# Kernel tuning notes

Hardware: AMD Instinct MI355X
Metric: run time of the kernel (lower is better)

The kernel has to match this reference:

```python
import jax, jax.numpy as jnp
import numpy as np

B, T, D, H = 4, 1024, 1024, 16
HD = D // H  # 64
EPS = 1e-5


def _layernorm(x, g, b):
    mu = jnp.mean(x, axis=-1, keepdims=True)
    var = jnp.mean(jnp.square(x - mu), axis=-1, keepdims=True)
    return (x - mu) * jax.lax.rsqrt(var + EPS) * g + b


def _apply_rope(x, cos, sin):
    # x: (B, H, T, HD); cos/sin: (T, HD//2)
    d = x.shape[-1] // 2
    x1, x2 = x[..., :d], x[..., d:]
    cos = cos[None, None]
    sin = sin[None, None]
    return jnp.concatenate([x1 * cos - x2 * sin, x1 * sin + x2 * cos], axis=-1)


def setup_inputs() -> dict:
    key = jax.random.key(0)
    ks = jax.random.split(key, 8)
    s = 0.02
    x = jax.random.normal(ks[0], (B, T, D), jnp.float32)
    # RoPE tables
    pos = jnp.arange(T, dtype=jnp.float32)
    inv_freq = 1.0 / (10000.0 ** (jnp.arange(HD // 2, dtype=jnp.float32) / (HD // 2)))
    ang = pos[:, None] * inv_freq[None, :]  # (T, HD//2)
    rope_cos, rope_sin = jnp.cos(ang), jnp.sin(ang)
    # causal mask: True = masked out (module does ~attn_mask before SDPA)
    attn_mask = jnp.triu(jnp.ones((T, T), dtype=bool), k=1)
    params = dict(
        ln1_g=jnp.ones((D,), jnp.float32), ln1_b=jnp.zeros((D,), jnp.float32),
        w_qkv=jax.random.normal(ks[1], (D, 3 * D), jnp.float32) * s,
        b_qkv=jnp.zeros((3 * D,), jnp.float32),
        w_out=jax.random.normal(ks[2], (D, D), jnp.float32) * s,
        b_out=jnp.zeros((D,), jnp.float32),
        ln2_g=jnp.ones((D,), jnp.float32), ln2_b=jnp.zeros((D,), jnp.float32),
        w1=jax.random.normal(ks[3], (D, 4 * D), jnp.float32) * s,
        b1=jnp.zeros((4 * D,), jnp.float32),
        w2=jax.random.normal(ks[4], (4 * D, D), jnp.float32) * s,
        b2=jnp.zeros((D,), jnp.float32),
    )
    return dict(x=x, attn_mask=attn_mask, rope_cos=rope_cos, rope_sin=rope_sin, **params)


def reference(x, attn_mask, rope_cos, rope_sin, ln1_g, ln1_b, w_qkv, b_qkv,
              w_out, b_out, ln2_g, ln2_b, w1, b1, w2, b2):
    b, t, d = x.shape
    h = _layernorm(x, ln1_g, ln1_b)
    qkv = (h @ w_qkv + b_qkv).reshape(b, t, 3, H, HD)
    q, k, v = jnp.transpose(qkv, (2, 0, 3, 1, 4))  # each (B, H, T, HD)
    q = _apply_rope(q, rope_cos, rope_sin)
    k = _apply_rope(k, rope_cos, rope_sin)
    scale = 1.0 / jnp.sqrt(jnp.asarray(HD, x.dtype))
    scores = jnp.einsum('bhqd,bhkd->bhqk', q, k) * scale
    allowed = ~attn_mask  # True = attend
    neg = jnp.finfo(scores.dtype).min
    scores = jnp.where(allowed[None, None], scores, neg)
    probs = jax.nn.softmax(scores, axis=-1)
    attn = jnp.einsum('bhqk,bhkd->bhqd', probs, v)
    attn = jnp.transpose(attn, (0, 2, 1, 3)).reshape(b, t, d)
    x = x + (attn @ w_out + b_out)
    h2 = _layernorm(x, ln2_g, ln2_b)
    mlp = jax.nn.gelu(h2 @ w1 + b1, approximate=False) @ w2 + b2
    return x + mlp
```

## Files before the change

### kernel.cpp

```cpp
#include <hip/hip_runtime.h>
#include <hip/hip_bf16.h>
#include <cstdint>


typedef __bf16 bf16x8_t __attribute__((ext_vector_type(8)));
typedef float  f32x4_t  __attribute__((ext_vector_type(4)));

#define MFMA16(a, b, c) __builtin_amdgcn_mfma_f32_16x16x32_bf16((a), (b), (c), 0, 0, 0)

static constexpr int Bb = 4, T = 1024, D = 1024, NH = 16, HD = 64;
static constexpr int ROWS = Bb * T;
static constexpr int QKVN = 3 * D;

__device__ __forceinline__ float bf2f(__hip_bfloat16 v) { return __bfloat162float(v); }
__device__ __forceinline__ ushort f2bfbits(float v) {
    __hip_bfloat16 h = __float2bfloat16(v);
    return *reinterpret_cast<ushort*>(&h);
}
__device__ __forceinline__ float loadf(const void* p, size_t i, int isb16) {
    return isb16 ? bf2f(((const __hip_bfloat16*)p)[i]) : ((const float*)p)[i];
}
__device__ __forceinline__ int dtype16(const void* gref) {
    return (((const unsigned*)gref)[0] & 0xFFFFu) != 0u;
}
__device__ __forceinline__ void gld_lds16(const __hip_bfloat16* g, __hip_bfloat16* l) {
    __builtin_amdgcn_global_load_lds(
        (const __attribute__((address_space(1))) void*)g,
        (__attribute__((address_space(3))) void*)l, 16, 0, 0);
}

__device__ __forceinline__ void trans_tile(const void* B, __hip_bfloat16* BT,
                                           int K, int N, int k0, int n0, int isb16) {
    __shared__ ushort t[64][65];
#pragma unroll
    for (int it = 0; it < 16; ++it) {
        int idx = threadIdx.x + it * 256;
        int r = idx >> 6, c = idx & 63;
        t[c][r] = f2bfbits(loadf(B, (size_t)(k0 + r) * N + n0 + c, isb16));
    }
    __syncthreads();
#pragma unroll
    for (int it = 0; it < 16; ++it) {
        int idx = threadIdx.x + it * 256;
        int r = idx >> 6, c = idx & 63;
        reinterpret_cast<ushort*>(BT)[(size_t)(n0 + r) * K + k0 + c] = t[r][c];
    }
}

__global__ __launch_bounds__(256) void transpose_k(const void* __restrict__ B,
                                                   __hip_bfloat16* __restrict__ BT,
                                                   const void* __restrict__ gref,
                                                   int K, int N) {
    trans_tile(B, BT, K, N, blockIdx.y * 64, blockIdx.x * 64, dtype16(gref));
}

__global__ __launch_bounds__(256) void megatrans_k(const void* w_qkv, const void* w_out,
                                                   const void* w1, const void* w2,
                                                   __hip_bfloat16* wqkvT, __hip_bfloat16* woutT,
                                                   __hip_bfloat16* w1T, __hip_bfloat16* w2T,
                                                   const void* __restrict__ gref) {
    const int isb16 = dtype16(gref);
    int bid = blockIdx.x;
    const void* src; __hip_bfloat16* dst; int K, N, l;
    if (bid < 768)       { src = w_qkv; dst = wqkvT; K = 1024; N = 3072; l = bid; }
    else if (bid < 1024) { src = w_out; dst = woutT; K = 1024; N = 1024; l = bid - 768; }
    else if (bid < 2048) { src = w1;    dst = w1T;   K = 1024; N = 4096; l = bid - 1024; }
    else                 { src = w2;    dst = w2T;   K = 4096; N = 1024; l = bid - 2048; }
    const int nb = N / 64;
    trans_tile(src, dst, K, N, (l / nb) * 64, (l % nb) * 64, isb16);
}

__global__ __launch_bounds__(256) void ln_k(const void* __restrict__ x,
                                            const void* __restrict__ g,
                                            const void* __restrict__ bt,
                                            __hip_bfloat16* __restrict__ out,
                                            const void* __restrict__ gref) {
    const int isb16 = dtype16(gref);
    const int row = blockIdx.x, tid = threadIdx.x;
    const int lane = tid & 63, w = tid >> 6;

    float v[4];
    if (isb16) {
        ushort4 raw = reinterpret_cast<const ushort4*>((const __hip_bfloat16*)x + (size_t)row * D)[tid];
        v[0] = __uint_as_float(((unsigned)raw.x) << 16);
        v[1] = __uint_as_float(((unsigned)raw.y) << 16);
        v[2] = __uint_as_float(((unsigned)raw.z) << 16);
        v[3] = __uint_as_float(((unsigned)raw.w) << 16);
    } else {
        float4 f = reinterpret_cast<const float4*>((const float*)x + (size_t)row * D)[tid];
        v[0] = f.x; v[1] = f.y; v[2] = f.z; v[3] = f.w;
    }

    float s1 = v[0] + v[1] + v[2] + v[3];
    float s2 = v[0] * v[0] + v[1] * v[1] + v[2] * v[2] + v[3] * v[3];
#pragma unroll
    for (int off = 32; off >= 1; off >>= 1) {
        s1 += __shfl_xor(s1, off, 64);
        s2 += __shfl_xor(s2, off, 64);
    }
    __shared__ float r1[4], r2[4];
    if (lane == 0) { r1[w] = s1; r2[w] = s2; }
    __syncthreads();
    float t1 = r1[0] + r1[1] + r1[2] + r1[3];
    float t2 = r2[0] + r2[1] + r2[2] + r2[3];
    float mu  = t1 * (1.0f / D);
    float var = t2 * (1.0f / D) - mu * mu;
    float rstd = rsqrtf(var + 1e-5f);

    const int c = tid * 4;
#pragma unroll
    for (int j = 0; j < 4; j++) {
        float gv = loadf(g, c + j, isb16), bv = loadf(bt, c + j, isb16);
        out[(size_t)row * D + c + j] = __float2bfloat16((v[j] - mu) * rstd * gv + bv);
    }
}

template <int MODE, bool SPLIT>
__global__ __launch_bounds__(256) void gemm_k(const __hip_bfloat16* __restrict__ A,
                                              const __hip_bfloat16* __restrict__ BT,
                                              const void* __restrict__ bias,
                                              void* __restrict__ C,
                                              const void* __restrict__ gref,
                                              int M, int N, int Kstride, int klen) {
    __shared__ __hip_bfloat16 LB[16384];

    const int tid  = threadIdx.x;
    const int lane = tid & 63, w = tid >> 6;
    const int quad = lane >> 4, l15 = lane & 15;
    const int n0 = blockIdx.x * 128, m0 = blockIdx.y * 128;
    const int wm = (w >> 1) * 64, wn = (w & 1) * 64;
    const int kbase = SPLIT ? blockIdx.z * klen : 0;

    const int srow = lane >> 2, skk = (lane & 3) * 8;
    const __hip_bfloat16* Ag = A  + (size_t)(m0 + w * 16 + srow) * Kstride + kbase + skk;
    const __hip_bfloat16* Bg = BT + (size_t)(n0 + w * 16 + srow) * Kstride + kbase + skk;
    const int lwb = (w * 16) * 32;

    f32x4_t acc[4][4] = {};

    gld_lds16(Ag,                LB + lwb);
    gld_lds16(Ag + 64 * Kstride, LB + lwb + 64 * 32);
    gld_lds16(Bg,                LB + 8192 + lwb);
    gld_lds16(Bg + 64 * Kstride, LB + 8192 + lwb + 64 * 32);
    __syncthreads();

    int p = 0;
    for (int k0 = 0; k0 < klen; k0 += 32) {
        if (k0 + 32 < klen) {
            __hip_bfloat16* An = LB + (p ^ 1) * 4096;
            __hip_bfloat16* Bn = LB + 8192 + (p ^ 1) * 4096;
            gld_lds16(Ag + k0 + 32,                An + lwb);
            gld_lds16(Ag + k0 + 32 + 64 * Kstride, An + lwb + 64 * 32);
            gld_lds16(Bg + k0 + 32,                Bn + lwb);
            gld_lds16(Bg + k0 + 32 + 64 * Kstride, Bn + lwb + 64 * 32);
        }

        const __hip_bfloat16* Ac = LB + p * 4096;
        const __hip_bfloat16* Bc = LB + 8192 + p * 4096;
        bf16x8_t af[4], bfr[4];
#pragma unroll
        for (int t = 0; t < 4; t++) {
            af[t]  = *reinterpret_cast<const bf16x8_t*>(&Ac[(wm + t * 16 + l15) * 32 + quad * 8]);
            bfr[t] = *reinterpret_cast<const bf16x8_t*>(&Bc[(wn + t * 16 + l15) * 32 + quad * 8]);
        }
#pragma unroll
        for (int i = 0; i < 4; i++)
#pragma unroll
            for (int j = 0; j < 4; j++)
                acc[i][j] = MFMA16(af[i], bfr[j], acc[i][j]);

        __syncthreads();
        p ^= 1;
    }

    __hip_bfloat16* Cb;
    if constexpr (SPLIT) {
        const int z = blockIdx.z;
        if (z == 0)      Cb = (__hip_bfloat16*)C;
        else if (z == 1) Cb = (__hip_bfloat16*)C + (size_t)M * N;
        else if (z == 2) Cb = (__hip_bfloat16*)const_cast<void*>(bias);
        else             Cb = (__hip_bfloat16*)const_cast<void*>(gref);
    } else {
        Cb = (__hip_bfloat16*)C;
    }
    const int isb16 = (MODE == 3) ? 0 : dtype16(gref);
    __hip_bfloat16* E = LB;
#pragma unroll
    for (int j = 0; j < 4; j++) {
        const int cc = wn + j * 16 + l15;
        const float bsv = (MODE == 3) ? 0.0f : loadf(bias, n0 + cc, isb16);
#pragma unroll
        for (int i = 0; i < 4; i++) {
            const int rbase = wm + i * 16 + quad * 4;
#pragma unroll
            for (int r = 0; r < 4; r++) {
                const int rr = rbase + r;
                float v = acc[i][j][r] + bsv;
                if constexpr (MODE == 2)
                    v = 0.5f * v * (1.0f + erff(v * 0.70710678118654752f));
                E[rr * 128 + ((cc + (((rr >> 2) & 7) << 4)) & 127)] = __float2bfloat16(v);
            }
        }
    }
    __syncthreads();
#pragma unroll
    for (int it = 0; it < 8; it++) {
        const int r = it * 16 + (tid >> 4), c = (tid & 15) * 8;
        const int cs = (c + (((r >> 2) & 7) << 4)) & 127;
        uint4 d = *reinterpret_cast<const uint4*>(&E[r * 128 + cs]);
        *reinterpret_cast<uint4*>(&Cb[(size_t)(m0 + r) * N + n0 + c]) = d;
    }
}

__global__ __launch_bounds__(256) void reduce4_k(const __hip_bfloat16* __restrict__ p0,
                                                 const __hip_bfloat16* __restrict__ p1,
                                                 const __hip_bfloat16* __restrict__ p2,
                                                 const __hip_bfloat16* __restrict__ p3,
                                                 const void* __restrict__ bias,
                                                 const void* __restrict__ res,
                                                 void* __restrict__ out,
                                                 const void* __restrict__ gref) {
    const int isb16 = dtype16(gref);
    const size_t i = ((size_t)blockIdx.x * 256 + threadIdx.x) * 4;
    ushort4 a = *reinterpret_cast<const ushort4*>(p0 + i);
    ushort4 b = *reinterpret_cast<const ushort4*>(p1 + i);
    ushort4 c = *reinterpret_cast<const ushort4*>(p2 + i);
    ushort4 d = *reinterpret_cast<const ushort4*>(p3 + i);
    const int col = (int)(i & (D - 1));
    float v[4];
    v[0] = __uint_as_float((unsigned)a.x << 16) + __uint_as_float((unsigned)b.x << 16)
         + __uint_as_float((unsigned)c.x << 16) + __uint_as_float((unsigned)d.x << 16);
    v[1] = __uint_as_float((unsigned)a.y << 16) + __uint_as_float((unsigned)b.y << 16)
         + __uint_as_float((unsigned)c.y << 16) + __uint_as_float((unsigned)d.y << 16);
    v[2] = __uint_as_float((unsigned)a.z << 16) + __uint_as_float((unsigned)b.z << 16)
         + __uint_as_float((unsigned)c.z << 16) + __uint_as_float((unsigned)d.z << 16);
    v[3] = __uint_as_float((unsigned)a.w << 16) + __uint_as_float((unsigned)b.w << 16)
         + __uint_as_float((unsigned)c.w << 16) + __uint_as_float((unsigned)d.w << 16);
#pragma unroll
    for (int j = 0; j < 4; j++)
        v[j] += loadf(bias, col + j, isb16) + loadf(res, i + j, isb16);
    if (isb16) {
        ushort4 o;
        o.x = f2bfbits(v[0]); o.y = f2bfbits(v[1]); o.z = f2bfbits(v[2]); o.w = f2bfbits(v[3]);
        *reinterpret_cast<ushort4*>((__hip_bfloat16*)out + i) = o;
    } else {
        float4 o = {v[0], v[1], v[2], v[3]};
        *reinterpret_cast<float4*>((float*)out + i) = o;
    }
}

__global__ __launch_bounds__(256) void gemm64_k(const __hip_bfloat16* __restrict__ A,
                                                const __hip_bfloat16* __restrict__ BT,
                                                const void* __restrict__ bias,
                                                const void* __restrict__ res,
                                                void* __restrict__ C,
                                                const void* __restrict__ gref,
                                                int M, int N, int K, int crow0) {
    __shared__ __hip_bfloat16 LB64[12288];

    const int tid  = threadIdx.x;
    const int lane = tid & 63, w = tid >> 6;
    const int quad = lane >> 4, l15 = lane & 15;
    const int n0 = blockIdx.x * 64, m0 = blockIdx.y * 128;
    const int wm = (w >> 1) * 64, wn = (w & 1) * 32;

    const int srow = lane >> 2, skk = (lane & 3) * 8;
    const __hip_bfloat16* Ag = A  + (size_t)(m0 + w * 16 + srow) * K + skk;
    const __hip_bfloat16* Bg = BT + (size_t)(n0 + w * 16 + srow) * K + skk;
    const int lwb = (w * 16) * 32;

    f32x4_t acc[4][2] = {};

    gld_lds16(Ag,          LB64 + lwb);
    gld_lds16(Ag + 64 * K, LB64 + lwb + 64 * 32);
    gld_lds16(Bg,          LB64 + 8192 + lwb);
    __syncthreads();

    int p = 0;
    for (int k0 = 0; k0 < K; k0 += 32) {
        if (k0 + 32 < K) {
            __hip_bfloat16* An = LB64 + (p ^ 1) * 4096;
            __hip_bfloat16* Bn = LB64 + 8192 + (p ^ 1) * 2048;
            gld_lds16(Ag + k0 + 32,          An + lwb);
            gld_lds16(Ag + k0 + 32 + 64 * K, An + lwb + 64 * 32);
            gld_lds16(Bg + k0 + 32,          Bn + lwb);
        }

        const __hip_bfloat16* Ac = LB64 + p * 4096;
        const __hip_bfloat16* Bc = LB64 + 8192 + p * 2048;
        bf16x8_t af[4], bfr[2];
#pragma unroll
        for (int t = 0; t < 4; t++)
            af[t]  = *reinterpret_cast<const bf16x8_t*>(&Ac[(wm + t * 16 + l15) * 32 + quad * 8]);
#pragma unroll
        for (int t = 0; t < 2; t++)
            bfr[t] = *reinterpret_cast<const bf16x8_t*>(&Bc[(wn + t * 16 + l15) * 32 + quad * 8]);
#pragma unroll
        for (int i = 0; i < 4; i++)
#pragma unroll
            for (int j = 0; j < 2; j++)
                acc[i][j] = MFMA16(af[i], bfr[j], acc[i][j]);

        __syncthreads();
        p ^= 1;
    }

    const int isb16 = dtype16(gref);
#pragma unroll
    for (int j = 0; j < 2; j++) {
        const int col = n0 + wn + j * 16 + l15;
        const float bsv = loadf(bias, col, isb16);
#pragma unroll
        for (int i = 0; i < 4; i++) {
            const int rbase = m0 + wm + i * 16 + quad * 4;
#pragma unroll
            for (int r = 0; r < 4; r++) {
                const size_t gr = (size_t)(crow0 + rbase + r);
                float v = acc[i][j][r] + bsv + loadf(res, gr * N + col, isb16);
                if (isb16) ((__hip_bfloat16*)C)[gr * N + col] = __float2bfloat16(v);
                else       ((float*)C)[gr * N + col] = v;
            }
        }
    }
}

__global__ __launch_bounds__(256) void ropevt_k(__hip_bfloat16* __restrict__ qkv,
                                                const void* __restrict__ rc,
                                                const void* __restrict__ rs,
                                                __hip_bfloat16* __restrict__ vT,
                                                const void* __restrict__ gref) {
    const int bid = blockIdx.x;
    if (bid < 8192) {
        const int isb16 = dtype16(gref);
        const int id = bid * 256 + threadIdx.x;
        const int d  = id & 31;
        const int h  = (id >> 5) & 15;
        const int t  = (id >> 9) & 1023;
        const int b  = id >> 19;
        const float c = loadf(rc, t * 32 + d, isb16);
        const float s = loadf(rs, t * 32 + d, isb16);
        __hip_bfloat16* base = qkv + ((size_t)(b * T + t)) * QKVN + h * HD + d;
        float x1 = bf2f(base[0]), x2 = bf2f(base[32]);
        base[0]  = __float2bfloat16((x1 * c - x2 * s) * 0.125f);
        base[32] = __float2bfloat16((x1 * s + x2 * c) * 0.125f);
        float y1 = bf2f(base[D]), y2 = bf2f(base[D + 32]);
        base[D]      = __float2bfloat16(y1 * c - y2 * s);
        base[D + 32] = __float2bfloat16(y1 * s + y2 * c);
    } else {
        __shared__ ushort t[64][65];
        const int l = bid - 8192;
        const int t0 = (l & 15) * 64, bh = l >> 4;
        const int b = bh >> 4, h = bh & 15;
        const __hip_bfloat16* src = qkv + ((size_t)b * T) * QKVN + 2 * D + h * HD;
#pragma unroll
        for (int it = 0; it < 16; ++it) {
            int idx = threadIdx.x + it * 256;
            int r = idx >> 6, d = idx & 63;
            t[d][r] = *reinterpret_cast<const ushort*>(src + (size_t)(t0 + r) * QKVN + d);
        }
        __syncthreads();
#pragma unroll
        for (int it = 0; it < 16; ++it) {
            int idx = threadIdx.x + it * 256;
            int r = idx >> 6, c = idx & 63;
            reinterpret_cast<ushort*>(vT)[((size_t)bh * 64 + r) * T + t0 + c] = t[r][c];
        }
    }
}

__global__ __launch_bounds__(256) void flash_k(const __hip_bfloat16* __restrict__ qkv,
                                               const __hip_bfloat16* __restrict__ vT,
                                               __hip_bfloat16* __restrict__ out) {
    __shared__ __hip_bfloat16 Qs[2][64 * 32];
    __shared__ __hip_bfloat16 Ks[2][2][64 * 32];
    __shared__ __hip_bfloat16 Vs[2][2][64 * 32];
    __shared__ __hip_bfloat16 Ps[4][2][16 * 32];

    const int tid = threadIdx.x;
    const int bid = blockIdx.x;
    const int qt = 15 - (bid >> 6);
    const int bh = bid & 63;
    const int b = bh >> 4, h = bh & 15;
    const int q0 = qt * 64;
    const int lane = tid & 63, w = tid >> 6, quad = lane >> 4, l15 = lane & 15;
    const int srow = lane >> 2, skk = (lane & 3) * 8;

    const __hip_bfloat16* qg = qkv + ((size_t)(b * T) + q0 + w * 16 + srow) * QKVN + h * HD + skk;
    const __hip_bfloat16* kg = qkv + ((size_t)(b * T) + w * 16 + srow) * QKVN + D + h * HD + skk;
    const __hip_bfloat16* vg = vT + ((size_t)bh * 64 + w * 16 + srow) * T + skk;

    gld_lds16(qg,      &Qs[0][(w * 16) * 32]);
    gld_lds16(qg + 32, &Qs[1][(w * 16) * 32]);
    gld_lds16(kg,      &Ks[0][0][(w * 16) * 32]);
    gld_lds16(kg + 32, &Ks[0][1][(w * 16) * 32]);
    gld_lds16(vg,      &Vs[0][0][(w * 16) * 32]);
    gld_lds16(vg + 32, &Vs[0][1][(w * 16) * 32]);
    __syncthreads();

    const bf16x8_t aq0 = *reinterpret_cast<const bf16x8_t*>(&Qs[0][(w * 16 + l15) * 32 + quad * 8]);
    const bf16x8_t aq1 = *reinterpret_cast<const bf16x8_t*>(&Qs[1][(w * 16 + l15) * 32 + quad * 8]);

    float m_run[4], l_run[4];
    f32x4_t o[4] = {};
#pragma unroll
    for (int i = 0; i < 4; i++) { m_run[i] = -1e30f; l_run[i] = 0.0f; }

    int p = 0;
    for (int kt = 0; kt <= qt; kt++) {
        if (kt < qt) {
            const size_t ko = (size_t)(kt + 1) * 64;
            gld_lds16(kg + ko * QKVN,      &Ks[p ^ 1][0][(w * 16) * 32]);
            gld_lds16(kg + ko * QKVN + 32, &Ks[p ^ 1][1][(w * 16) * 32]);
            gld_lds16(vg + ko,             &Vs[p ^ 1][0][(w * 16) * 32]);
            gld_lds16(vg + ko + 32,        &Vs[p ^ 1][1][(w * 16) * 32]);
        }

        f32x4_t s[4];
#pragma unroll
        for (int c = 0; c < 4; c++) {
            f32x4_t z = {};
            bf16x8_t k0f = *reinterpret_cast<const bf16x8_t*>(&Ks[p][0][(c * 16 + l15) * 32 + quad * 8]);
            bf16x8_t k1f = *reinterpret_cast<const bf16x8_t*>(&Ks[p][1][(c * 16 + l15) * 32 + quad * 8]);
            z = MFMA16(aq0, k0f, z);
            z = MFMA16(aq1, k1f, z);
            s[c] = z;
        }

        if (kt == qt) {
#pragma unroll
            for (int c = 0; c < 4; c++)
#pragma unroll
                for (int i = 0; i < 4; i++) {
                    int rr = w * 16 + quad * 4 + i;
                    int cc = c * 16 + l15;
                    if (cc > rr) s[c][i] = -1e30f;
                }
        }

        float mnew[4], alpha[4];
#pragma unroll
        for (int i = 0; i < 4; i++) {
            float mx = fmaxf(fmaxf(s[0][i], s[1][i]), fmaxf(s[2][i], s[3][i]));
#pragma unroll
            for (int off = 1; off < 16; off <<= 1) mx = fmaxf(mx, __shfl_xor(mx, off, 64));
            mnew[i] = fmaxf(m_run[i], mx);
            alpha[i] = __expf(m_run[i] - mnew[i]);
            m_run[i] = mnew[i];
        }
#pragma unroll
        for (int c = 0; c < 4; c++)
#pragma unroll
            for (int i = 0; i < 4; i++) s[c][i] = __expf(s[c][i] - mnew[i]);
#pragma unroll
        for (int i = 0; i < 4; i++) {
            float sm = s[0][i] + s[1][i] + s[2][i] + s[3][i];
#pragma unroll
            for (int off = 1; off < 16; off <<= 1) sm += __shfl_xor(sm, off, 64);
            l_run[i] = l_run[i] * alpha[i] + sm;
#pragma unroll
            for (int od = 0; od < 4; od++) o[od][i] *= alpha[i];
        }

#pragma unroll
        for (int c = 0; c < 4; c++)
#pragma unroll
            for (int i = 0; i < 4; i++)
                Ps[w][c >> 1][(quad * 4 + i) * 32 + (c & 1) * 16 + l15] =
                    __float2bfloat16(s[c][i]);

        bf16x8_t ap0 = *reinterpret_cast<const bf16x8_t*>(&Ps[w][0][l15 * 32 + quad * 8]);
        bf16x8_t ap1 = *reinterpret_cast<const bf16x8_t*>(&Ps[w][1][l15 * 32 + quad * 8]);
#pragma unroll
        for (int od = 0; od < 4; od++) {
            bf16x8_t v0f = *reinterpret_cast<const bf16x8_t*>(&Vs[p][0][(od * 16 + l15) * 32 + quad * 8]);
            bf16x8_t v1f = *reinterpret_cast<const bf16x8_t*>(&Vs[p][1][(od * 16 + l15) * 32 + quad * 8]);
            o[od] = MFMA16(ap0, v0f, o[od]);
            o[od] = MFMA16(ap1, v1f, o[od]);
        }

        __syncthreads();
        p ^= 1;
    }

#pragma unroll
    for (int od = 0; od < 4; od++)
#pragma unroll
        for (int i = 0; i < 4; i++) {
            int row = q0 + w * 16 + quad * 4 + i;
            int col = h * HD + od * 16 + l15;
            float v = o[od][i] / l_run[i];
            out[((size_t)b * T + row) * D + col] = __float2bfloat16(v);
        }
}

extern "C" void kernel_launch(void* const* d_in, const int* in_sizes, int n_in,
                              void* d_out, int out_size, void* d_ws, size_t ws_size,
                              hipStream_t stream) {
    const int o = (in_sizes[1] == T * (HD / 2)) ? 1 : 2;
    const void* x     = d_in[0];
    const void* rc    = d_in[o + 0];
    const void* rs    = d_in[o + 1];
    const void* ln1g  = d_in[o + 2];
    const void* ln1b  = d_in[o + 3];
    const void* w_qkv = d_in[o + 4];
    const void* b_qkv = d_in[o + 5];
    const void* w_out = d_in[o + 6];
    const void* b_out = d_in[o + 7];
    const void* ln2g  = d_in[o + 8];
    const void* ln2b  = d_in[o + 9];
    const void* w1    = d_in[o + 10];
    const void* b1    = d_in[o + 11];
    const void* w2    = d_in[o + 12];
    const void* b2    = d_in[o + 13];

    char* ws = (char*)d_ws;
    const size_t MB = 1024 * 1024;

    if (ws_size >= 72 * MB + 256) {
        __hip_bfloat16* bufA  = (__hip_bfloat16*)(ws + 256);
        __hip_bfloat16* qkvb  = (__hip_bfloat16*)(ws + 8 * MB + 256);
        __hip_bfloat16* vTb   = (__hip_bfloat16*)(ws + 32 * MB + 256);
        __hip_bfloat16* mid   = qkvb;
        __hip_bfloat16* wqkvT = (__hip_bfloat16*)(ws + 40 * MB + 256);
        __hip_bfloat16* woutT = (__hip_bfloat16*)(ws + 46 * MB + 256);
        __hip_bfloat16* w1T   = (__hip_bfloat16*)(ws + 48 * MB + 256);
        __hip_bfloat16* w2T   = (__hip_bfloat16*)(ws + 56 * MB + 256);
        __hip_bfloat16* part0 = (__hip_bfloat16*)(ws + 40 * MB + 256);
        __hip_bfloat16* part2 = (__hip_bfloat16*)(ws + 64 * MB + 256);
        __hip_bfloat16* part1 = (__hip_bfloat16*)(ws + 48 * MB + 256);
        __hip_bfloat16* part3 = bufA;

        megatrans_k<<<3072, 256, 0, stream>>>(w_qkv, w_out, w1, w2,
                                              wqkvT, woutT, w1T, w2T, ln1g);
        ln_k<<<ROWS, 256, 0, stream>>>(x, ln1g, ln1b, bufA, ln1g);
        gemm_k<0, false><<<dim3(QKVN / 128, ROWS / 128), 256, 0, stream>>>(
            bufA, wqkvT, b_qkv, qkvb, ln1g, ROWS, QKVN, D, D);
        ropevt_k<<<8192 + 1024, 256, 0, stream>>>(qkvb, rc, rs, vTb, ln1g);
        flash_k<<<16 * Bb * NH, 256, 0, stream>>>(qkvb, vTb, bufA);
        gemm64_k<<<dim3(D / 64, ROWS / 128), 256, 0, stream>>>(bufA, woutT, b_out, x,
                                                               d_out, ln1g, ROWS, D, D, 0);
        ln_k<<<ROWS, 256, 0, stream>>>(d_out, ln2g, ln2b, bufA, ln1g);
        gemm_k<2, false><<<dim3(4 * D / 128, ROWS / 128), 256, 0, stream>>>(
            bufA, w1T, b1, mid, ln1g, ROWS, 4 * D, D, D);
        gemm_k<3, true><<<dim3(D / 128, ROWS / 128, 4), 256, 0, stream>>>(
            mid, w2T, part2, part0, part3, ROWS, D, 4 * D, D);
        reduce4_k<<<(ROWS * D) / (256 * 4), 256, 0, stream>>>(part0, part1, part2, part3,
                                                              b2, d_out, d_out, ln1g);
    } else {
        __hip_bfloat16* bufA  = (__hip_bfloat16*)(ws + 256);
        __hip_bfloat16* qkvb  = (__hip_bfloat16*)(ws + 8 * MB + 256);
        __hip_bfloat16* wqkvT = (__hip_bfloat16*)(ws + 32 * MB + 256);
        __hip_bfloat16* vTb   = (__hip_bfloat16*)(ws + 32 * MB + 256);
        __hip_bfloat16* woutT = (__hip_bfloat16*)(ws + 8 * MB + 256);
        __hip_bfloat16* w1T   = (__hip_bfloat16*)(ws + 8 * MB + 256);
        __hip_bfloat16* w2T   = (__hip_bfloat16*)(ws + 16 * MB + 256);
        __hip_bfloat16* mid   = (__hip_bfloat16*)(ws + 24 * MB + 256);

        transpose_k<<<dim3(QKVN / 64, D / 64), 256, 0, stream>>>(w_qkv, wqkvT, ln1g, D, QKVN);
        ln_k<<<ROWS, 256, 0, stream>>>(x, ln1g, ln1b, bufA, ln1g);
        gemm_k<0, false><<<dim3(QKVN / 128, ROWS / 128), 256, 0, stream>>>(
            bufA, wqkvT, b_qkv, qkvb, ln1g, ROWS, QKVN, D, D);
        ropevt_k<<<8192 + 1024, 256, 0, stream>>>(qkvb, rc, rs, vTb, ln1g);
        flash_k<<<16 * Bb * NH, 256, 0, stream>>>(qkvb, vTb, bufA);
        transpose_k<<<dim3(D / 64, D / 64), 256, 0, stream>>>(w_out, woutT, ln1g, D, D);
        gemm64_k<<<dim3(D / 64, ROWS / 128), 256, 0, stream>>>(bufA, woutT, b_out, x,
                                                               d_out, ln1g, ROWS, D, D, 0);
        ln_k<<<ROWS, 256, 0, stream>>>(d_out, ln2g, ln2b, bufA, ln1g);
        transpose_k<<<dim3(4 * D / 64, D / 64), 256, 0, stream>>>(w1, w1T, ln1g, D, 4 * D);
        transpose_k<<<dim3(D / 64, 4 * D / 64), 256, 0, stream>>>(w2, w2T, ln1g, 4 * D, D);
        for (int c = 0; c < 2; c++) {
            const int ro = c * 2048;
            gemm_k<2, false><<<dim3(4 * D / 128, 2048 / 128), 256, 0, stream>>>(
                bufA + (size_t)ro * D, w1T, b1, mid, ln1g, 2048, 4 * D, D, D);
            gemm64_k<<<dim3(D / 64, 2048 / 128), 256, 0, stream>>>(mid, w2T, b2, d_out,
                                                                   d_out, ln1g, 2048, D, 4 * D, ro);
        }
    }
}
```

Before: 399.8 us.

## Add 256x256-tile 512-thread GEMM with 4-stage LDS pipeline for QKV and MLP

```diff
diff --git a/kernel.cpp b/kernel.cpp
--- a/kernel.cpp
+++ b/kernel.cpp
@@ -112,6 +112,130 @@
     for (int j = 0; j < 4; j++) {
         float gv = loadf(g, c + j, isb16), bv = loadf(bt, c + j, isb16);
         out[(size_t)row * D + c + j] = __float2bfloat16((v[j] - mu) * rstd * gv + bv);
+    }
+}
+
+template <int MODE, bool SPLIT>
+__global__ __launch_bounds__(512, 2) void gemm256_k(const __hip_bfloat16* __restrict__ A,
+                                                    const __hip_bfloat16* __restrict__ BT,
+                                                    const void* __restrict__ bias,
+                                                    void* __restrict__ C,
+                                                    const void* __restrict__ gref,
+                                                    int M, int N, int Kstride, int klen) {
+    extern __shared__ __hip_bfloat16 LDSb[];
+
+    const int tid  = threadIdx.x;
+    const int lane = tid & 63, w = tid >> 6;
+    const int quad = lane >> 4, l15 = lane & 15;
+    const int n0 = blockIdx.x * 256, m0 = blockIdx.y * 256;
+    const int wmL = (w >> 2) * 128;
+    const int wnL = (w & 3) * 64;
+    const int kbase = SPLIT ? blockIdx.z * klen : 0;
+    const int NT = klen >> 5;
+
+    const int L0 = w * 1024 + lane * 16;
+    const int L1 = L0 + 8192;
+    const int r0 = L0 >> 6,  k0e = ((L0 & 63) ^ (((L0 >> 9) & 1) << 5)) >> 1;
+    const int r1 = L1 >> 6,  k1e = ((L1 & 63) ^ (((L1 >> 9) & 1) << 5)) >> 1;
+    const __hip_bfloat16* AgS0 = A  + (size_t)(m0 + r0) * Kstride + kbase + k0e;
+    const __hip_bfloat16* AgS1 = A  + (size_t)(m0 + r1) * Kstride + kbase + k1e;
+    const __hip_bfloat16* BgS0 = BT + (size_t)(n0 + r0) * Kstride + kbase + k0e;
+    const __hip_bfloat16* BgS1 = BT + (size_t)(n0 + r1) * Kstride + kbase + k1e;
+    const int ldst0 = w * 512, ldst1 = w * 512 + 4096;
+
+    const int kofs = (quad * 8) ^ ((l15 & 8) << 1);
+
+    f32x4_t acc[8][4] = {};
+
+#pragma unroll
+    for (int t = 0; t < 3; ++t) {
+        __hip_bfloat16* sA = LDSb + t * 8192;
+        __hip_bfloat16* sB = LDSb + 32768 + t * 8192;
+        const int ko = t * 32;
+        gld_lds16(AgS0 + ko, sA + ldst0);
+        gld_lds16(AgS1 + ko, sA + ldst1);
+        gld_lds16(BgS0 + ko, sB + ldst0);
+        gld_lds16(BgS1 + ko, sB + ldst1);
+    }
+    asm volatile("s_waitcnt vmcnt(8)" ::: "memory");
+    __builtin_amdgcn_s_barrier();
+    __builtin_amdgcn_sched_barrier(0);
+
+    for (int t = 0; t < NT; ++t) {
+        if (t) {
+            if (t + 2 < NT)      { asm volatile("s_waitcnt vmcnt(8)" ::: "memory"); }
+            else if (t + 1 < NT) { asm volatile("s_waitcnt vmcnt(4)" ::: "memory"); }
+            else                 { asm volatile("s_waitcnt vmcnt(0)" ::: "memory"); }
+            __builtin_amdgcn_s_barrier();
+            __builtin_amdgcn_sched_barrier(0);
+        }
+        if (t + 3 < NT) {
+            const int sl = (t + 3) & 3;
+            __hip_bfloat16* sA = LDSb + sl * 8192;
+            __hip_bfloat16* sB = LDSb + 32768 + sl * 8192;
+            const int ko = (t + 3) * 32;
+            gld_lds16(AgS0 + ko, sA + ldst0);
+            gld_lds16(AgS1 + ko, sA + ldst1);
+            gld_lds16(BgS0 + ko, sB + ldst0);
+            gld_lds16(BgS1 + ko, sB + ldst1);
+        }
+
+        const __hip_bfloat16* sA = LDSb + (t & 3) * 8192;
+        const __hip_bfloat16* sB = LDSb + 32768 + (t & 3) * 8192;
+        bf16x8_t a[8], b[4];
+#pragma unroll
+        for (int mf = 0; mf < 8; ++mf)
+            a[mf] = *reinterpret_cast<const bf16x8_t*>(&sA[(wmL + mf * 16 + l15) * 32 + kofs]);
+#pragma unroll
+        for (int nf = 0; nf < 4; ++nf)
+            b[nf] = *reinterpret_cast<const bf16x8_t*>(&sB[(wnL + nf * 16 + l15) * 32 + kofs]);
+        __builtin_amdgcn_s_setprio(1);
+#pragma unroll
+        for (int mf = 0; mf < 8; ++mf)
+#pragma unroll
+            for (int nf = 0; nf < 4; ++nf)
+                acc[mf][nf] = MFMA16(a[mf], b[nf], acc[mf][nf]);
+        __builtin_amdgcn_s_setprio(0);
+    }
+
+    __syncthreads();
+
+    __hip_bfloat16* Cb;
+    if constexpr (SPLIT) {
+        const int z = blockIdx.z;
+        if (z == 0)      Cb = (__hip_bfloat16*)C;
+        else if (z == 1) Cb = (__hip_bfloat16*)C + (size_t)M * N;
+        else if (z == 2) Cb = (__hip_bfloat16*)const_cast<void*>(bias);
+        else             Cb = (__hip_bfloat16*)const_cast<void*>(gref);
+    } else {
+        Cb = (__hip_bfloat16*)C;
+    }
+    const int isb16 = (MODE == 3) ? 0 : dtype16(gref);
+    __hip_bfloat16* E = LDSb;
+#pragma unroll
+    for (int nf = 0; nf < 4; ++nf) {
+        const int cc = wnL + nf * 16 + l15;
+        const float bsv = (MODE == 3) ? 0.0f : loadf(bias, n0 + cc, isb16);
+#pragma unroll
+        for (int mf = 0; mf < 8; ++mf) {
+            const int rbase = wmL + mf * 16 + quad * 4;
+#pragma unroll
+            for (int r = 0; r < 4; ++r) {
+                const int rr = rbase + r;
+                float v = acc[mf][nf][r] + bsv;
+                if constexpr (MODE == 2)
+                    v = 0.5f * v * (1.0f + erff(v * 0.70710678118654752f));
+                E[rr * 256 + ((cc + (((rr >> 2) & 15) << 4)) & 255)] = __float2bfloat16(v);
+            }
+        }
+    }
+    __syncthreads();
+#pragma unroll
+    for (int it = 0; it < 16; ++it) {
+        const int r = it * 16 + (tid >> 5), c = (tid & 31) * 8;
+        const int cs = (c + (((r >> 2) & 15) << 4)) & 255;
+        uint4 d = *reinterpret_cast<const uint4*>(&E[r * 256 + cs]);
+        *reinterpret_cast<uint4*>(&Cb[(size_t)(m0 + r) * N + n0 + c]) = d;
     }
 }
 
@@ -516,6 +640,17 @@
     char* ws = (char*)d_ws;
     const size_t MB = 1024 * 1024;
 
+    static bool attr_done = false;
+    if (!attr_done) {
+        hipFuncSetAttribute(reinterpret_cast<const void*>(&gemm256_k<0, false>),
+                            hipFuncAttributeMaxDynamicSharedMemorySize, 131072);
+        hipFuncSetAttribute(reinterpret_cast<const void*>(&gemm256_k<2, false>),
+                            hipFuncAttributeMaxDynamicSharedMemorySize, 131072);
+        hipFuncSetAttribute(reinterpret_cast<const void*>(&gemm256_k<3, true>),
+                            hipFuncAttributeMaxDynamicSharedMemorySize, 131072);
+        attr_done = true;
+    }
+
     if (ws_size >= 72 * MB + 256) {
         __hip_bfloat16* bufA  = (__hip_bfloat16*)(ws + 256);
         __hip_bfloat16* qkvb  = (__hip_bfloat16*)(ws + 8 * MB + 256);
@@ -533,16 +668,16 @@
         megatrans_k<<<3072, 256, 0, stream>>>(w_qkv, w_out, w1, w2,
                                               wqkvT, woutT, w1T, w2T, ln1g);
         ln_k<<<ROWS, 256, 0, stream>>>(x, ln1g, ln1b, bufA, ln1g);
-        gemm_k<0, false><<<dim3(QKVN / 128, ROWS / 128), 256, 0, stream>>>(
+        gemm256_k<0, false><<<dim3(QKVN / 256, ROWS / 256), 512, 131072, stream>>>(
             bufA, wqkvT, b_qkv, qkvb, ln1g, ROWS, QKVN, D, D);
         ropevt_k<<<8192 + 1024, 256, 0, stream>>>(qkvb, rc, rs, vTb, ln1g);
         flash_k<<<16 * Bb * NH, 256, 0, stream>>>(qkvb, vTb, bufA);
         gemm64_k<<<dim3(D / 64, ROWS / 128), 256, 0, stream>>>(bufA, woutT, b_out, x,
                                                                d_out, ln1g, ROWS, D, D, 0);
         ln_k<<<ROWS, 256, 0, stream>>>(d_out, ln2g, ln2b, bufA, ln1g);
-        gemm_k<2, false><<<dim3(4 * D / 128, ROWS / 128), 256, 0, stream>>>(
+        gemm256_k<2, false><<<dim3(4 * D / 256, ROWS / 256), 512, 131072, stream>>>(
             bufA, w1T, b1, mid, ln1g, ROWS, 4 * D, D, D);
-        gemm_k<3, true><<<dim3(D / 128, ROWS / 128, 4), 256, 0, stream>>>(
+        gemm256_k<3, true><<<dim3(D / 256, ROWS / 256, 4), 512, 131072, stream>>>(
             mid, w2T, part2, part0, part3, ROWS, D, 4 * D, D);
         reduce4_k<<<(ROWS * D) / (256 * 4), 256, 0, stream>>>(part0, part1, part2, part3,
                                                               b2, d_out, d_out, ln1g);
```

Measured after the change: 372.8 us. -6.7%, faster.

## Add 256x256-tile GEMM kernel with XCD-aware block swizzle for QKV and MLP

Applied to the files above, without the earlier changes.

```diff
diff --git a/kernel.cpp b/kernel.cpp
--- a/kernel.cpp
+++ b/kernel.cpp
@@ -112,6 +112,109 @@
     for (int j = 0; j < 4; j++) {
         float gv = loadf(g, c + j, isb16), bv = loadf(bt, c + j, isb16);
         out[(size_t)row * D + c + j] = __float2bfloat16((v[j] - mu) * rstd * gv + bv);
+    }
+}
+
+template <int MODE, bool SPLIT>
+__global__ __launch_bounds__(1024, 4) void gemm256_k(const __hip_bfloat16* __restrict__ A,
+                                                     const __hip_bfloat16* __restrict__ BT,
+                                                     const void* __restrict__ bias,
+                                                     void* __restrict__ C,
+                                                     const void* __restrict__ gref,
+                                                     int M, int N, int Kstride, int klen) {
+    __shared__ __hip_bfloat16 LB[32768];
+
+    const int tid  = threadIdx.x;
+    const int lane = tid & 63, w = tid >> 6;
+    const int quad = lane >> 4, l15 = lane & 15;
+
+    const int gx = gridDim.x;
+    const int nwg = gx * gridDim.y;
+    const int id = (int)blockIdx.y * gx + (int)blockIdx.x;
+    const int cpx = nwg >> 3;
+    const int sid = (id & 7) * cpx + (id >> 3);
+    const int n0 = (sid % gx) * 256, m0 = (sid / gx) * 256;
+
+    const int wmL = (w >> 3) * 128;
+    const int wnL = (w & 7) * 32;
+    const int kbase = SPLIT ? blockIdx.z * klen : 0;
+    const int NT = klen >> 5;
+
+    const int gcol = 8 * ((lane & 3) ^ ((lane >> 2) & 3));
+    const __hip_bfloat16* AgS = A  + (size_t)(m0 + w * 16 + (lane >> 2)) * Kstride + kbase + gcol;
+    const __hip_bfloat16* BgS = BT + (size_t)(n0 + w * 16 + (lane >> 2)) * Kstride + kbase + gcol;
+    const int ldst = w * 512;
+
+    const int cSw = (quad * 8) ^ ((l15 & 3) << 3);
+
+    f32x4_t acc[8][2] = {};
+
+    gld_lds16(AgS, LB + ldst);
+    gld_lds16(BgS, LB + 16384 + ldst);
+    __syncthreads();
+
+    for (int t = 0; t < NT; ++t) {
+        if (t + 1 < NT) {
+            const int sl = (t + 1) & 1;
+            gld_lds16(AgS + (t + 1) * 32, LB + sl * 8192 + ldst);
+            gld_lds16(BgS + (t + 1) * 32, LB + 16384 + sl * 8192 + ldst);
+        }
+        const __hip_bfloat16* As = LB + (t & 1) * 8192;
+        const __hip_bfloat16* Bs = LB + 16384 + (t & 1) * 8192;
+        bf16x8_t b0 = *reinterpret_cast<const bf16x8_t*>(&Bs[(wnL + l15) * 32 + cSw]);
+        bf16x8_t b1 = *reinterpret_cast<const bf16x8_t*>(&Bs[(wnL + 16 + l15) * 32 + cSw]);
+#pragma unroll
+        for (int mf = 0; mf < 8; ++mf) {
+            bf16x8_t a = *reinterpret_cast<const bf16x8_t*>(&As[(wmL + mf * 16 + l15) * 32 + cSw]);
+            acc[mf][0] = MFMA16(a, b0, acc[mf][0]);
+            acc[mf][1] = MFMA16(a, b1, acc[mf][1]);
+        }
+        __syncthreads();
+    }
+
+    __hip_bfloat16* Cb;
+    if constexpr (SPLIT) {
+        const int z = blockIdx.z;
+        if (z == 0)      Cb = (__hip_bfloat16*)C;
+        else if (z == 1) Cb = (__hip_bfloat16*)C + (size_t)M * N;
+        else if (z == 2) Cb = (__hip_bfloat16*)const_cast<void*>(bias);
+        else             Cb = (__hip_bfloat16*)const_cast<void*>(gref);
+    } else {
+        Cb = (__hip_bfloat16*)C;
+    }
+    const int isb16 = (MODE == 3) ? 0 : dtype16(gref);
+    __hip_bfloat16* E = LB;
+    const int myh = w >> 3;
+#pragma unroll
+    for (int h = 0; h < 2; ++h) {
+        __syncthreads();
+        if (myh == h) {
+#pragma unroll
+            for (int nf = 0; nf < 2; ++nf) {
+                const int cc = wnL + nf * 16 + l15;
+                const float bsv = (MODE == 3) ? 0.0f : loadf(bias, n0 + cc, isb16);
+#pragma unroll
+                for (int mf = 0; mf < 8; ++mf) {
+                    const int rbase = mf * 16 + quad * 4;
+#pragma unroll
+                    for (int r = 0; r < 4; ++r) {
+                        const int rr = rbase + r;
+                        float v = acc[mf][nf][r] + bsv;
+                        if constexpr (MODE == 2)
+                            v = 0.5f * v * (1.0f + erff(v * 0.70710678118654752f));
+                        E[rr * 256 + ((cc + (((rr >> 2) & 15) << 4)) & 255)] = __float2bfloat16(v);
+                    }
+                }
+            }
+        }
+        __syncthreads();
+#pragma unroll
+        for (int it = 0; it < 4; ++it) {
+            const int r = it * 32 + (tid >> 5), c = (tid & 31) * 8;
+            const int cs = (c + (((r >> 2) & 15) << 4)) & 255;
+            uint4 d = *reinterpret_cast<const uint4*>(&E[r * 256 + cs]);
+            *reinterpret_cast<uint4*>(&Cb[(size_t)(m0 + h * 128 + r) * N + n0 + c]) = d;
+        }
     }
 }
 
@@ -533,16 +636,16 @@
         megatrans_k<<<3072, 256, 0, stream>>>(w_qkv, w_out, w1, w2,
                                               wqkvT, woutT, w1T, w2T, ln1g);
         ln_k<<<ROWS, 256, 0, stream>>>(x, ln1g, ln1b, bufA, ln1g);
-        gemm_k<0, false><<<dim3(QKVN / 128, ROWS / 128), 256, 0, stream>>>(
+        gemm256_k<0, false><<<dim3(QKVN / 256, ROWS / 256), 1024, 0, stream>>>(
             bufA, wqkvT, b_qkv, qkvb, ln1g, ROWS, QKVN, D, D);
         ropevt_k<<<8192 + 1024, 256, 0, stream>>>(qkvb, rc, rs, vTb, ln1g);
         flash_k<<<16 * Bb * NH, 256, 0, stream>>>(qkvb, vTb, bufA);
         gemm64_k<<<dim3(D / 64, ROWS / 128), 256, 0, stream>>>(bufA, woutT, b_out, x,
                                                                d_out, ln1g, ROWS, D, D, 0);
         ln_k<<<ROWS, 256, 0, stream>>>(d_out, ln2g, ln2b, bufA, ln1g);
-        gemm_k<2, false><<<dim3(4 * D / 128, ROWS / 128), 256, 0, stream>>>(
+        gemm256_k<2, false><<<dim3(4 * D / 256, ROWS / 256), 1024, 0, stream>>>(
             bufA, w1T, b1, mid, ln1g, ROWS, 4 * D, D, D);
-        gemm_k<3, true><<<dim3(D / 128, ROWS / 128, 4), 256, 0, stream>>>(
+        gemm256_k<3, true><<<dim3(D / 256, ROWS / 256, 4), 1024, 0, stream>>>(
             mid, w2T, part2, part0, part3, ROWS, D, 4 * D, D);
         reduce4_k<<<(ROWS * D) / (256 * 4), 256, 0, stream>>>(part0, part1, part2, part3,
                                                               b2, d_out, d_out, ln1g);
```

New measurement: 444.1 us. 1.11x slower.
